# Kernel optimization log

Hardware: AMD Instinct MI355X
Metric: run time of the kernel (lower is better)

## Reference

```python
import jax, jax.numpy as jnp
import numpy as np

B, T, C, H = 4, 2048, 1024, 16
D = C // H  # head dim = 64

def setup_inputs() -> dict:
    key = jax.random.key(0)
    ks = jax.random.split(key, 9)
    s = 1.0 / np.sqrt(C)
    return {
        "x":  jax.random.normal(ks[0], (B, T, C), jnp.float32),
        "Wq": jax.random.normal(ks[1], (C, C), jnp.float32) * s,
        "bq": jax.random.normal(ks[2], (C,), jnp.float32) * 0.02,
        "Wk": jax.random.normal(ks[3], (C, C), jnp.float32) * s,
        "bk": jax.random.normal(ks[4], (C,), jnp.float32) * 0.02,
        "Wv": jax.random.normal(ks[5], (C, C), jnp.float32) * s,
        "bv": jax.random.normal(ks[6], (C,), jnp.float32) * 0.02,
        "Wp": jax.random.normal(ks[7], (C, C), jnp.float32) * s,
        "bp": jax.random.normal(ks[8], (C,), jnp.float32) * 0.02,
    }

def reference(x, Wq, bq, Wk, bk, Wv, bv, Wp, bp):
    Bx, Tx, Cx = x.shape
    # projections; PyTorch Linear computes x @ W.T + b
    q = (x @ Wq.T + bq).reshape(Bx, Tx, H, D).transpose(0, 2, 1, 3)  # [B,H,T,D]
    k = (x @ Wk.T + bk).reshape(Bx, Tx, H, D).transpose(0, 2, 1, 3)
    v = (x @ Wv.T + bv).reshape(Bx, Tx, H, D).transpose(0, 2, 1, 3)
    att = jnp.einsum('bhtd,bhsd->bhts', q, k) * (1.0 / np.sqrt(D))  # [B,H,T,T]
    causal = jnp.tril(jnp.ones((Tx, Tx), bool))
    att = jnp.where(causal[None, None], att, -jnp.inf)
    att = jax.nn.softmax(att, axis=-1)
    y = jnp.einsum('bhts,bhsd->bhtd', att, v)  # [B,H,T,D]
    y = y.transpose(0, 2, 1, 3).reshape(Bx, Tx, Cx)
    return y @ Wp.T + bp
```

## Files before the change

kernel.cpp:

```cpp
#include <hip/hip_runtime.h>
#include <hip/hip_bf16.h>
#include <math.h>

static constexpr int Bn = 4, Tlen = 2048, Cdim = 1024, Hn = 16, Dh = 64;
static constexpr int Mtot = Bn * Tlen;

typedef __attribute__((ext_vector_type(8)))  short    s16x8;
typedef __attribute__((ext_vector_type(4)))  float    f32x4;
typedef __attribute__((ext_vector_type(16))) float    f32x16;
typedef __attribute__((ext_vector_type(2)))  unsigned u32x2;
typedef unsigned short u16;

#define QSCALE 0.18033688011112042f

__device__ __forceinline__ u16 f2bf(float f) {
    union { float f; unsigned u; } x; x.f = f;
    unsigned r = x.u + 0x7FFFu + ((x.u >> 16) & 1u);
    return (u16)(r >> 16);
}
__device__ __forceinline__ unsigned cvtpk(float lo, float hi) {
    unsigned r;
    asm("v_cvt_pk_bf16_f32 %0, %1, %2" : "=v"(r) : "v"(lo), "v"(hi));
    return r;
}
__device__ __forceinline__ void gload_lds16(const void* g, void* l) {
    __builtin_amdgcn_global_load_lds(
        (const __attribute__((address_space(1))) void*)g,
        (__attribute__((address_space(3))) void*)l, 16, 0, 0);
}

__global__ __launch_bounds__(256) void cvt_bf16(const float* __restrict__ in,
                                                u16* __restrict__ out) {
    size_t i = (size_t)(blockIdx.x * 256 + threadIdx.x) * 8;
    float4 a = *(const float4*)(in + i);
    float4 b = *(const float4*)(in + i + 4);
    s16x8 o;
    o[0] = (short)f2bf(a.x); o[1] = (short)f2bf(a.y);
    o[2] = (short)f2bf(a.z); o[3] = (short)f2bf(a.w);
    o[4] = (short)f2bf(b.x); o[5] = (short)f2bf(b.y);
    o[6] = (short)f2bf(b.z); o[7] = (short)f2bf(b.w);
    *(s16x8*)(out + i) = o;
}

template <int MODE, int NB>
__global__ __launch_bounds__(512, 4) void gemm8w(const u16* __restrict__ A,
                                                 const u16* __restrict__ Bm,
                                                 const float* __restrict__ bq,
                                                 const float* __restrict__ bk,
                                                 const float* __restrict__ bv,
                                                 void* __restrict__ out0,
                                                 u16* __restrict__ vt) {
    constexpr int K = Cdim;
    constexpr int NKT = K / 32;
    __shared__ u16 As[3][128 * 32];
    __shared__ u16 Bs[3][256 * 32];

    const int f  = blockIdx.x;
    const int f2 = (f & 7) * (8 * NB) + (f >> 3);
    const int bm = f2 / NB, bn = f2 % NB;
    const int m0 = bm * 128, n0g = bn * 256;

    const int tid = threadIdx.x, lane = tid & 63, w = tid >> 6;
    const int wm = w >> 2, wn = w & 3;
    const int rowA = lane & 15, kg = lane >> 4;

    const int srow  = w * 16 + (lane >> 2);
    const int scolA = (((lane & 3) ^ (srow & 3)) * 8);
    const u16* Ab  = A  + (size_t)(m0 + srow) * K + scolA;
    const u16* Bb0 = Bm + (size_t)(n0g + srow) * K + scolA;
    const u16* Bb1 = Bm + (size_t)(n0g + 128 + srow) * K + scolA;

#define STAGE_T(KT, BUF)                                              \
    do {                                                              \
        const int k0_ = (KT) * 32;                                    \
        gload_lds16(Ab  + k0_, &As[BUF][w * 512]);                    \
        gload_lds16(Bb0 + k0_, &Bs[BUF][w * 512]);                    \
        gload_lds16(Bb1 + k0_, &Bs[BUF][4096 + w * 512]);             \
    } while (0)

    const int fswz = ((kg ^ (rowA & 3)) * 8);
    const int aoff = (wm * 64 + rowA) * 32 + fswz;
    const int boff = (wn * 64 + rowA) * 32 + fswz;

    f32x4 acc[4][4] = {};

    STAGE_T(0, 0);
    STAGE_T(1, 1);
    asm volatile("s_waitcnt vmcnt(3)" ::: "memory");
    __builtin_amdgcn_s_barrier();

    for (int kt = 0; kt < NKT; ++kt) {
        const int cur = kt % 3;
        s16x8 af[4], bf[4];
#pragma unroll
        for (int i = 0; i < 4; ++i) {
            af[i] = *(const s16x8*)&As[cur][aoff + i * 512];
            bf[i] = *(const s16x8*)&Bs[cur][boff + i * 512];
        }
        if (kt + 2 < NKT) STAGE_T(kt + 2, (kt + 2) % 3);
        __builtin_amdgcn_s_barrier();

        __builtin_amdgcn_s_setprio(1);
#pragma unroll
        for (int mf = 0; mf < 4; ++mf)
#pragma unroll
            for (int nf = 0; nf < 4; ++nf)
                acc[mf][nf] = __builtin_amdgcn_mfma_f32_16x16x32_bf16(
                    af[mf], bf[nf], acc[mf][nf], 0, 0, 0);
        __builtin_amdgcn_s_setprio(0);

        if (kt + 2 < NKT) asm volatile("s_waitcnt vmcnt(3)" ::: "memory");
        else              asm volatile("s_waitcnt vmcnt(0)" ::: "memory");
        __builtin_amdgcn_s_barrier();
    }
#undef STAGE_T

    const int which = (MODE == 1) ? (n0g >> 10) : 0;
    const int n0 = n0g & 1023;
    const float* bias = (MODE == 0) ? bq : (which == 0 ? bq : (which == 1 ? bk : bv));
    const float osc = (MODE == 1 && which == 0) ? QSCALE : 1.0f;
    float bb[4];
#pragma unroll
    for (int nf = 0; nf < 4; ++nf) bb[nf] = bias[n0 + wn * 64 + nf * 16 + rowA];

    if (MODE == 0) {
        float* C = (float*)out0;
#pragma unroll
        for (int mf = 0; mf < 4; ++mf)
#pragma unroll
            for (int nf = 0; nf < 4; ++nf)
#pragma unroll
                for (int r = 0; r < 4; ++r) {
                    size_t row = m0 + wm * 64 + mf * 16 + kg * 4 + r;
                    size_t col = n0 + wn * 64 + nf * 16 + rowA;
                    C[row * 1024 + col] = acc[mf][nf][r] + bb[nf];
                }
    } else if (which < 2) {
        u16* C = (u16*)out0 + (size_t)which * ((size_t)Mtot * Cdim);
#pragma unroll
        for (int mf = 0; mf < 4; ++mf)
#pragma unroll
            for (int nf = 0; nf < 4; ++nf)
#pragma unroll
                for (int r = 0; r < 4; ++r) {
                    float val = (acc[mf][nf][r] + bb[nf]) * osc;
                    size_t row = m0 + wm * 64 + mf * 16 + kg * 4 + r;
                    size_t col = n0 + wn * 64 + nf * 16 + rowA;
                    C[row * 1024 + col] = f2bf(val);
                }
    } else {
#pragma unroll
        for (int mf = 0; mf < 4; ++mf)
#pragma unroll
            for (int nf = 0; nf < 4; ++nf) {
                int hd = n0 + wn * 64 + nf * 16 + rowA;
                size_t row0 = m0 + wm * 64 + mf * 16 + kg * 4;
                int bi = (int)(row0 >> 11), t0 = (int)(row0 & 2047);
                union { u16 h[4]; u32x2 d; } pk;
#pragma unroll
                for (int r = 0; r < 4; ++r) pk.h[r] = f2bf(acc[mf][nf][r] + bb[nf]);
                *(u32x2*)(vt + ((size_t)bi * 1024 + hd) * Tlen + t0) = pk.d;
            }
    }
}

__global__ __launch_bounds__(256, 4) void attn_mfma(const u16* __restrict__ q,
                                                    const u16* __restrict__ k,
                                                    const u16* __restrict__ vt,
                                                    u16* y) {
    const int fid = blockIdx.x;
    const int qt = 15 - (fid >> 6);
    const int rem = fid & 63;
    const int h = rem & 15, b = rem >> 4;
    const int tid = threadIdx.x, lane = tid & 63, w = tid >> 6;
    const int qlane = lane & 31, hi = lane >> 5;
    __shared__ u16 Ks[2][64 * 64];
    __shared__ u16 Vs[2][64 * 64];

    const int q0 = qt * 128;
    const int qrow_g = q0 + w * 32 + qlane;

    const u16* qrow = q + ((size_t)(b * Tlen) + qrow_g) * Cdim + h * Dh;
    s16x8 qf[4];
#pragma unroll
    for (int s = 0; s < 4; ++s)
        qf[s] = *(const s16x8*)(qrow + s * 16 + hi * 8);

    const u16* kbase = k + ((size_t)(b * Tlen)) * Cdim + h * Dh;
    const u16* vbase = vt + ((size_t)(b * Hn + h)) * (size_t)(Dh * Tlen);

    const int g0row = tid >> 3;
    const int g1row = g0row + 32;
    const int gc0 = (((tid) & 7) ^ (g0row & 7)) * 8;
    const int gc1 = (((tid) & 7) ^ (g1row & 7)) * 8;

#define STAGE(JT, BUF)                                                              \
    do {                                                                            \
        const u16* kb2 = kbase + (size_t)((JT) * 64) * Cdim;                        \
        const u16* vb2 = vbase + (JT) * 64;                                         \
        gload_lds16(kb2 + (size_t)g0row * Cdim + gc0, &Ks[BUF][w * 512]);           \
        gload_lds16(kb2 + (size_t)g1row * Cdim + gc1, &Ks[BUF][2048 + w * 512]);    \
        gload_lds16(vb2 + (size_t)g0row * Tlen + gc0, &Vs[BUF][w * 512]);           \
        gload_lds16(vb2 + (size_t)g1row * Tlen + gc1, &Vs[BUF][2048 + w * 512]);    \
    } while (0)

    STAGE(0, 0);

    f32x16 o0, o1;
#pragma unroll
    for (int r = 0; r < 16; ++r) { o0[r] = 0.f; o1[r] = 0.f; }
    float m_i = -INFINITY, l_i = 0.f;

    const int njt = 2 * qt + 2;
    const int jtmax = 2 * qt + (w >> 1);
    const int swz = (qlane & 7);

    for (int jt = 0; jt < njt; ++jt) {
        const int cur = jt & 1;
        if (jt + 1 < njt) {
            STAGE(jt + 1, cur ^ 1);
            asm volatile("s_waitcnt vmcnt(4)" ::: "memory");
        } else {
            asm volatile("s_waitcnt vmcnt(0)" ::: "memory");
        }
        __builtin_amdgcn_s_barrier();

        if (jt <= jtmax) {
            const u16* kc = &Ks[cur][0];
            const u16* vc = &Vs[cur][0];
            f32x16 sA, sB;
#pragma unroll
            for (int r = 0; r < 16; ++r) { sA[r] = 0.f; sB[r] = 0.f; }
            __builtin_amdgcn_s_setprio(1);
#pragma unroll
            for (int s = 0; s < 4; ++s) {
                const int g8 = ((2 * s + hi) ^ swz) * 8;
                s16x8 k0 = *(const s16x8*)&kc[qlane * 64 + g8];
                s16x8 k1 = *(const s16x8*)&kc[(qlane + 32) * 64 + g8];
                sA = __builtin_amdgcn_mfma_f32_32x32x16_bf16(k0, qf[s], sA, 0, 0, 0);
                sB = __builtin_amdgcn_mfma_f32_32x32x16_bf16(k1, qf[s], sB, 0, 0, 0);
            }
            __builtin_amdgcn_s_setprio(0);

            if (jt * 64 + 63 > q0 + w * 32) {
#pragma unroll
                for (int r = 0; r < 16; ++r) {
                    int kv = jt * 64 + (r & 3) + 8 * (r >> 2) + 4 * hi;
                    if (kv > qrow_g)      sA[r] = -INFINITY;
                    if (kv + 32 > qrow_g) sB[r] = -INFINITY;
                }
            }
            float pm = -INFINITY;
#pragma unroll
            for (int r = 0; r < 16; ++r) pm = fmaxf(pm, fmaxf(sA[r], sB[r]));
            pm = fmaxf(pm, __shfl_xor(pm, 32));
            const bool skip = (bool)__all(pm <= m_i + 8.0f);
            float nm = m_i, sc = 1.0f;
            if (!skip) {
                nm = fmaxf(m_i, pm);
                sc = exp2f(m_i - nm);
                m_i = nm;
            }
            float ps = 0.f;
#pragma unroll
            for (int r = 0; r < 16; ++r) {
                sA[r] = exp2f(sA[r] - nm); ps += sA[r];
                sB[r] = exp2f(sB[r] - nm); ps += sB[r];
            }
            ps += __shfl_xor(ps, 32);
            if (!skip) {
                l_i = l_i * sc + ps;
#pragma unroll
                for (int r = 0; r < 16; ++r) { o0[r] *= sc; o1[r] *= sc; }
            } else {
                l_i += ps;
            }

            s16x8 pf[4];
            auto packsub = [&](const f32x16& sv, s16x8* out) {
#pragma unroll
                for (int t = 0; t < 2; ++t) {
                    unsigned X = cvtpk(sv[8 * t + 0], sv[8 * t + 1]);
                    unsigned Z = cvtpk(sv[8 * t + 2], sv[8 * t + 3]);
                    unsigned Y = cvtpk(sv[8 * t + 4], sv[8 * t + 5]);
                    unsigned W = cvtpk(sv[8 * t + 6], sv[8 * t + 7]);
                    unsigned U0 = hi ? Y : X, V0 = hi ? X : Y;
                    unsigned U1 = hi ? W : Z, V1 = hi ? Z : W;
                    unsigned S0 = (unsigned)__shfl_xor((int)V0, 32);
                    unsigned S1 = (unsigned)__shfl_xor((int)V1, 32);
                    union { unsigned u[4]; s16x8 v; } fr;
                    fr.u[0] = hi ? S0 : U0;
                    fr.u[1] = hi ? S1 : U1;
                    fr.u[2] = hi ? U0 : S0;
                    fr.u[3] = hi ? U1 : S1;
                    out[t] = fr.v;
                }
            };
            packsub(sA, pf);
            packsub(sB, pf + 2);

            __builtin_amdgcn_s_setprio(1);
#pragma unroll
            for (int t = 0; t < 4; ++t) {
                const int g8 = ((2 * t + hi) ^ swz) * 8;
                s16x8 v0 = *(const s16x8*)&vc[qlane * 64 + g8];
                s16x8 v1 = *(const s16x8*)&vc[(qlane + 32) * 64 + g8];
                o0 = __builtin_amdgcn_mfma_f32_32x32x16_bf16(v0, pf[t], o0, 0, 0, 0);
                o1 = __builtin_amdgcn_mfma_f32_32x32x16_bf16(v1, pf[t], o1, 0, 0, 0);
            }
            __builtin_amdgcn_s_setprio(0);
        }
        asm volatile("" ::: "memory");
        __builtin_amdgcn_s_barrier();
    }
#undef STAGE

    float inv = 1.f / l_i;
    u16* yrow = y + ((size_t)(b * Tlen) + qrow_g) * Cdim + h * Dh;
#pragma unroll
    for (int g2 = 0; g2 < 4; ++g2) {
        u32x2 st;
        st[0] = cvtpk(o0[4 * g2 + 0] * inv, o0[4 * g2 + 1] * inv);
        st[1] = cvtpk(o0[4 * g2 + 2] * inv, o0[4 * g2 + 3] * inv);
        *(u32x2*)(yrow + 8 * g2 + 4 * hi) = st;
        st[0] = cvtpk(o1[4 * g2 + 0] * inv, o1[4 * g2 + 1] * inv);
        st[1] = cvtpk(o1[4 * g2 + 2] * inv, o1[4 * g2 + 3] * inv);
        *(u32x2*)(yrow + 32 + 8 * g2 + 4 * hi) = st;
    }
}

extern "C" void kernel_launch(void* const* d_in, const int* in_sizes, int n_in,
                              void* d_out, int out_size, void* d_ws, size_t ws_size,
                              hipStream_t stream) {
    const float* x  = (const float*)d_in[0];
    const float* Wq = (const float*)d_in[1];
    const float* bq = (const float*)d_in[2];
    const float* Wk = (const float*)d_in[3];
    const float* bk = (const float*)d_in[4];
    const float* Wv = (const float*)d_in[5];
    const float* bv = (const float*)d_in[6];
    const float* Wp = (const float*)d_in[7];
    const float* bp = (const float*)d_in[8];
    float* out = (float*)d_out;

    const size_t plane = (size_t)Mtot * Cdim;
    const size_t wsz   = (size_t)Cdim * Cdim;
    u16* xb    = (u16*)d_ws;
    u16* wqkvb = xb + plane;
    u16* wpb   = wqkvb + 3 * wsz;
    u16* qb    = wpb + wsz;
    u16* kb    = qb + plane;
    u16* vtb   = kb + plane;

    cvt_bf16<<<plane / 2048, 256, 0, stream>>>(x, xb);
    cvt_bf16<<<wsz / 2048, 256, 0, stream>>>(Wq, wqkvb);
    cvt_bf16<<<wsz / 2048, 256, 0, stream>>>(Wk, wqkvb + wsz);
    cvt_bf16<<<wsz / 2048, 256, 0, stream>>>(Wv, wqkvb + 2 * wsz);
    cvt_bf16<<<wsz / 2048, 256, 0, stream>>>(Wp, wpb);

    gemm8w<1, 12><<<dim3(768), 512, 0, stream>>>(xb, wqkvb, bq, bk, bv, qb, vtb);

    attn_mfma<<<dim3(1024), 256, 0, stream>>>(qb, kb, vtb, qb);

    gemm8w<0, 4><<<dim3(256), 512, 0, stream>>>(qb, wpb, bp, bp, bp, out, nullptr);
}
```

Measured before the change: 183.1 us.

## Pair causal query tiles per block and use permlane32 swap for P packing

Each attention block now processes two query tiles, qt and 15-qt, one after the other, so every block does the same amount of causal work, and the grid is halved to 512 blocks. The bf16 P-fragment repacking now uses v_permlane32_swap instead of shuffles and selects. The row sum stays per half-wave until the end, with a single cross-half add at normalisation. The first QK MFMA now accumulates from a zero vector instead of zeroing the accumulators. The aim is to remove tail imbalance and cut per-tile VALU and shuffle work, at the cost of fewer blocks in flight and no overlap between the two halves' prologue loads.

New measurement: 183.8 us. Within noise of the previous version (+0.4%).

```diff
diff --git a/kernel.cpp b/kernel.cpp
--- a/kernel.cpp
+++ b/kernel.cpp
@@ -22,6 +22,9 @@
     unsigned r;
     asm("v_cvt_pk_bf16_f32 %0, %1, %2" : "=v"(r) : "v"(lo), "v"(hi));
     return r;
+}
+__device__ __forceinline__ void lane32swap(unsigned& a, unsigned& b) {
+    asm("v_permlane32_swap_b32 %0, %1" : "+v"(a), "+v"(b));
 }
 __device__ __forceinline__ void gload_lds16(const void* g, void* l) {
     __builtin_amdgcn_global_load_lds(
@@ -169,22 +172,13 @@
                                                     const u16* __restrict__ vt,
                                                     u16* y) {
     const int fid = blockIdx.x;
-    const int qt = 15 - (fid >> 6);
+    const int pidx = fid >> 6;
     const int rem = fid & 63;
     const int h = rem & 15, b = rem >> 4;
     const int tid = threadIdx.x, lane = tid & 63, w = tid >> 6;
     const int qlane = lane & 31, hi = lane >> 5;
     __shared__ u16 Ks[2][64 * 64];
     __shared__ u16 Vs[2][64 * 64];
-
-    const int q0 = qt * 128;
-    const int qrow_g = q0 + w * 32 + qlane;
-
-    const u16* qrow = q + ((size_t)(b * Tlen) + qrow_g) * Cdim + h * Dh;
-    s16x8 qf[4];
-#pragma unroll
-    for (int s = 0; s < 4; ++s)
-        qf[s] = *(const s16x8*)(qrow + s * 16 + hi * 8);
 
     const u16* kbase = k + ((size_t)(b * Tlen)) * Cdim + h * Dh;
     const u16* vbase = vt + ((size_t)(b * Hn + h)) * (size_t)(Dh * Tlen);
@@ -204,129 +198,142 @@
         gload_lds16(vb2 + (size_t)g1row * Tlen + gc1, &Vs[BUF][2048 + w * 512]);    \
     } while (0)
 
-    STAGE(0, 0);
-
-    f32x16 o0, o1;
-#pragma unroll
-    for (int r = 0; r < 16; ++r) { o0[r] = 0.f; o1[r] = 0.f; }
-    float m_i = -INFINITY, l_i = 0.f;
-
-    const int njt = 2 * qt + 2;
-    const int jtmax = 2 * qt + (w >> 1);
+    f32x16 zv;
+#pragma unroll
+    for (int r = 0; r < 16; ++r) zv[r] = 0.f;
     const int swz = (qlane & 7);
 
-    for (int jt = 0; jt < njt; ++jt) {
-        const int cur = jt & 1;
-        if (jt + 1 < njt) {
-            STAGE(jt + 1, cur ^ 1);
-            asm volatile("s_waitcnt vmcnt(4)" ::: "memory");
-        } else {
-            asm volatile("s_waitcnt vmcnt(0)" ::: "memory");
+    for (int half = 0; half < 2; ++half) {
+        const int qt = half ? (15 - pidx) : pidx;
+        const int q0 = qt * 128;
+        const int qrow_g = q0 + w * 32 + qlane;
+
+        const u16* qrow = q + ((size_t)(b * Tlen) + qrow_g) * Cdim + h * Dh;
+        s16x8 qf[4];
+#pragma unroll
+        for (int s = 0; s < 4; ++s)
+            qf[s] = *(const s16x8*)(qrow + s * 16 + hi * 8);
+
+        STAGE(0, 0);
+
+        f32x16 o0 = zv, o1 = zv;
+        float m_i = -INFINITY, l_i = 0.f;
+
+        const int njt = 2 * qt + 2;
+        const int jtmax = 2 * qt + (w >> 1);
+
+        for (int jt = 0; jt < njt; ++jt) {
+            const int cur = jt & 1;
+            if (jt + 1 < njt) {
+                STAGE(jt + 1, cur ^ 1);
+                asm volatile("s_waitcnt vmcnt(4)" ::: "memory");
+            } else {
+                asm volatile("s_waitcnt vmcnt(0)" ::: "memory");
+            }
+            __builtin_amdgcn_s_barrier();
+
+            if (jt <= jtmax) {
+                const u16* kc = &Ks[cur][0];
+                const u16* vc = &Vs[cur][0];
+                f32x16 sA, sB;
+                __builtin_amdgcn_s_setprio(1);
+                {
+                    const int g8 = (hi ^ swz) * 8;
+                    s16x8 k0 = *(const s16x8*)&kc[qlane * 64 + g8];
+                    s16x8 k1 = *(const s16x8*)&kc[(qlane + 32) * 64 + g8];
+                    sA = __builtin_amdgcn_mfma_f32_32x32x16_bf16(k0, qf[0], zv, 0, 0, 0);
+                    sB = __builtin_amdgcn_mfma_f32_32x32x16_bf16(k1, qf[0], zv, 0, 0, 0);
+                }
+#pragma unroll
+                for (int s = 1; s < 4; ++s) {
+                    const int g8 = ((2 * s + hi) ^ swz) * 8;
+                    s16x8 k0 = *(const s16x8*)&kc[qlane * 64 + g8];
+                    s16x8 k1 = *(const s16x8*)&kc[(qlane + 32) * 64 + g8];
+                    sA = __builtin_amdgcn_mfma_f32_32x32x16_bf16(k0, qf[s], sA, 0, 0, 0);
+                    sB = __builtin_amdgcn_mfma_f32_32x32x16_bf16(k1, qf[s], sB, 0, 0, 0);
+                }
+                __builtin_amdgcn_s_setprio(0);
+
+                if (jt * 64 + 63 > q0 + w * 32) {
+#pragma unroll
+                    for (int r = 0; r < 16; ++r) {
+                        int kv = jt * 64 + (r & 3) + 8 * (r >> 2) + 4 * hi;
+                        if (kv > qrow_g)      sA[r] = -INFINITY;
+                        if (kv + 32 > qrow_g) sB[r] = -INFINITY;
+                    }
+                }
+                float pm = -INFINITY;
+#pragma unroll
+                for (int r = 0; r < 16; ++r) pm = fmaxf(pm, fmaxf(sA[r], sB[r]));
+                pm = fmaxf(pm, __shfl_xor(pm, 32));
+                const bool skip = (bool)__all(pm <= m_i + 8.0f);
+                float nm = m_i, sc = 1.0f;
+                if (!skip) {
+                    nm = fmaxf(m_i, pm);
+                    sc = exp2f(m_i - nm);
+                    m_i = nm;
+                }
+                float ps = 0.f;
+#pragma unroll
+                for (int r = 0; r < 16; ++r) {
+                    sA[r] = exp2f(sA[r] - nm); ps += sA[r];
+                    sB[r] = exp2f(sB[r] - nm); ps += sB[r];
+                }
+                if (!skip) {
+                    l_i = l_i * sc + ps;
+#pragma unroll
+                    for (int r = 0; r < 16; ++r) { o0[r] *= sc; o1[r] *= sc; }
+                } else {
+                    l_i += ps;
+                }
+
+                s16x8 pf[4];
+                auto packsub = [&](const f32x16& sv, s16x8* out) {
+#pragma unroll
+                    for (int t = 0; t < 2; ++t) {
+                        unsigned X = cvtpk(sv[8 * t + 0], sv[8 * t + 1]);
+                        unsigned Z = cvtpk(sv[8 * t + 2], sv[8 * t + 3]);
+                        unsigned Y = cvtpk(sv[8 * t + 4], sv[8 * t + 5]);
+                        unsigned W = cvtpk(sv[8 * t + 6], sv[8 * t + 7]);
+                        lane32swap(X, Y);
+                        lane32swap(Z, W);
+                        union { unsigned u[4]; s16x8 v; } fr;
+                        fr.u[0] = X; fr.u[1] = Z; fr.u[2] = Y; fr.u[3] = W;
+                        out[t] = fr.v;
+                    }
+                };
+                packsub(sA, pf);
+                packsub(sB, pf + 2);
+
+                __builtin_amdgcn_s_setprio(1);
+#pragma unroll
+                for (int t = 0; t < 4; ++t) {
+                    const int g8 = ((2 * t + hi) ^ swz) * 8;
+                    s16x8 v0 = *(const s16x8*)&vc[qlane * 64 + g8];
+                    s16x8 v1 = *(const s16x8*)&vc[(qlane + 32) * 64 + g8];
+                    o0 = __builtin_amdgcn_mfma_f32_32x32x16_bf16(v0, pf[t], o0, 0, 0, 0);
+                    o1 = __builtin_amdgcn_mfma_f32_32x32x16_bf16(v1, pf[t], o1, 0, 0, 0);
+                }
+                __builtin_amdgcn_s_setprio(0);
+            }
+            asm volatile("" ::: "memory");
+            __builtin_amdgcn_s_barrier();
         }
-        __builtin_amdgcn_s_barrier();
-
-        if (jt <= jtmax) {
-            const u16* kc = &Ks[cur][0];
-            const u16* vc = &Vs[cur][0];
-            f32x16 sA, sB;
-#pragma unroll
-            for (int r = 0; r < 16; ++r) { sA[r] = 0.f; sB[r] = 0.f; }
-            __builtin_amdgcn_s_setprio(1);
-#pragma unroll
-            for (int s = 0; s < 4; ++s) {
-                const int g8 = ((2 * s + hi) ^ swz) * 8;
-                s16x8 k0 = *(const s16x8*)&kc[qlane * 64 + g8];
-                s16x8 k1 = *(const s16x8*)&kc[(qlane + 32) * 64 + g8];
-                sA = __builtin_amdgcn_mfma_f32_32x32x16_bf16(k0, qf[s], sA, 0, 0, 0);
-                sB = __builtin_amdgcn_mfma_f32_32x32x16_bf16(k1, qf[s], sB, 0, 0, 0);
-            }
-            __builtin_amdgcn_s_setprio(0);
-
-            if (jt * 64 + 63 > q0 + w * 32) {
-#pragma unroll
-                for (int r = 0; r < 16; ++r) {
-                    int kv = jt * 64 + (r & 3) + 8 * (r >> 2) + 4 * hi;
-                    if (kv > qrow_g)      sA[r] = -INFINITY;
-                    if (kv + 32 > qrow_g) sB[r] = -INFINITY;
-                }
-            }
-            float pm = -INFINITY;
-#pragma unroll
-            for (int r = 0; r < 16; ++r) pm = fmaxf(pm, fmaxf(sA[r], sB[r]));
-            pm = fmaxf(pm, __shfl_xor(pm, 32));
-            const bool skip = (bool)__all(pm <= m_i + 8.0f);
-            float nm = m_i, sc = 1.0f;
-            if (!skip) {
-                nm = fmaxf(m_i, pm);
-                sc = exp2f(m_i - nm);
-                m_i = nm;
-            }
-            float ps = 0.f;
-#pragma unroll
-            for (int r = 0; r < 16; ++r) {
-                sA[r] = exp2f(sA[r] - nm); ps += sA[r];
-                sB[r] = exp2f(sB[r] - nm); ps += sB[r];
-            }
-            ps += __shfl_xor(ps, 32);
-            if (!skip) {
-                l_i = l_i * sc + ps;
-#pragma unroll
-                for (int r = 0; r < 16; ++r) { o0[r] *= sc; o1[r] *= sc; }
-            } else {
-                l_i += ps;
-            }
-
-            s16x8 pf[4];
-            auto packsub = [&](const f32x16& sv, s16x8* out) {
-#pragma unroll
-                for (int t = 0; t < 2; ++t) {
-                    unsigned X = cvtpk(sv[8 * t + 0], sv[8 * t + 1]);
-                    unsigned Z = cvtpk(sv[8 * t + 2], sv[8 * t + 3]);
-                    unsigned Y = cvtpk(sv[8 * t + 4], sv[8 * t + 5]);
-                    unsigned W = cvtpk(sv[8 * t + 6], sv[8 * t + 7]);
-                    unsigned U0 = hi ? Y : X, V0 = hi ? X : Y;
-                    unsigned U1 = hi ? W : Z, V1 = hi ? Z : W;
-                    unsigned S0 = (unsigned)__shfl_xor((int)V0, 32);
-                    unsigned S1 = (unsigned)__shfl_xor((int)V1, 32);
-                    union { unsigned u[4]; s16x8 v; } fr;
-                    fr.u[0] = hi ? S0 : U0;
-                    fr.u[1] = hi ? S1 : U1;
-                    fr.u[2] = hi ? U0 : S0;
-                    fr.u[3] = hi ? U1 : S1;
-                    out[t] = fr.v;
-                }
-            };
-            packsub(sA, pf);
-            packsub(sB, pf + 2);
-
-            __builtin_amdgcn_s_setprio(1);
-#pragma unroll
-            for (int t = 0; t < 4; ++t) {
-                const int g8 = ((2 * t + hi) ^ swz) * 8;
-                s16x8 v0 = *(const s16x8*)&vc[qlane * 64 + g8];
-                s16x8 v1 = *(const s16x8*)&vc[(qlane + 32) * 64 + g8];
-                o0 = __builtin_amdgcn_mfma_f32_32x32x16_bf16(v0, pf[t], o0, 0, 0, 0);
-                o1 = __builtin_amdgcn_mfma_f32_32x32x16_bf16(v1, pf[t], o1, 0, 0, 0);
-            }
-            __builtin_amdgcn_s_setprio(0);
+
+        float inv = 1.f / (l_i + __shfl_xor(l_i, 32));
+        u16* yrow = y + ((size_t)(b * Tlen) + qrow_g) * Cdim + h * Dh;
+#pragma unroll
+        for (int g2 = 0; g2 < 4; ++g2) {
+            u32x2 st;
+            st[0] = cvtpk(o0[4 * g2 + 0] * inv, o0[4 * g2 + 1] * inv);
+            st[1] = cvtpk(o0[4 * g2 + 2] * inv, o0[4 * g2 + 3] * inv);
+            *(u32x2*)(yrow + 8 * g2 + 4 * hi) = st;
+            st[0] = cvtpk(o1[4 * g2 + 0] * inv, o1[4 * g2 + 1] * inv);
+            st[1] = cvtpk(o1[4 * g2 + 2] * inv, o1[4 * g2 + 3] * inv);
+            *(u32x2*)(yrow + 32 + 8 * g2 + 4 * hi) = st;
         }
-        asm volatile("" ::: "memory");
-        __builtin_amdgcn_s_barrier();
     }
 #undef STAGE
-
-    float inv = 1.f / l_i;
-    u16* yrow = y + ((size_t)(b * Tlen) + qrow_g) * Cdim + h * Dh;
-#pragma unroll
-    for (int g2 = 0; g2 < 4; ++g2) {
-        u32x2 st;
-        st[0] = cvtpk(o0[4 * g2 + 0] * inv, o0[4 * g2 + 1] * inv);
-        st[1] = cvtpk(o0[4 * g2 + 2] * inv, o0[4 * g2 + 3] * inv);
-        *(u32x2*)(yrow + 8 * g2 + 4 * hi) = st;
-        st[0] = cvtpk(o1[4 * g2 + 0] * inv, o1[4 * g2 + 1] * inv);
-        st[1] = cvtpk(o1[4 * g2 + 2] * inv, o1[4 * g2 + 3] * inv);
-        *(u32x2*)(yrow + 32 + 8 * g2 + 4 * hi) = st;
-    }
 }
 
 extern "C" void kernel_launch(void* const* d_in, const int* in_sizes, int n_in,
@@ -360,7 +367,7 @@
 
     gemm8w<1, 12><<<dim3(768), 512, 0, stream>>>(xb, wqkvb, bq, bk, bv, qb, vtb);
 
-    attn_mfma<<<dim3(1024), 256, 0, stream>>>(qb, kb, vtb, qb);
+    attn_mfma<<<dim3(512), 256, 0, stream>>>(qb, kb, vtb, qb);
 
     gemm8w<0, 4><<<dim3(256), 512, 0, stream>>>(qb, wpb, bp, bp, bp, out, nullptr);
 }
```
